# Optimization experiments

Measured on AMD Instinct MI355X. Metric: run time of the kernel, lower is better.

The kernel has to match this reference:

```python
import jax, jax.numpy as jnp
import numpy as np

B_SZ, SEQ, D_MODEL, D_STATE, KSIZE = 8, 4096, 1024, 64, 64
DT_MIN, DT_MAX = 0.001, 0.1


def setup_inputs() -> dict:
    key = jax.random.key(0)
    k1, k2, k3, k4 = jax.random.split(key, 4)
    u = jax.random.normal(k1, (B_SZ, SEQ, D_MODEL), dtype=jnp.float32)
    # HiPPO-like init: A = -(n+1)
    A = -(jnp.arange(D_STATE, dtype=jnp.float32) + 1.0)
    Bp = 0.01 * jax.random.normal(k2, (D_STATE, D_MODEL), dtype=jnp.float32)
    Cp = 0.01 * jax.random.normal(k3, (D_MODEL, D_STATE), dtype=jnp.float32)
    Dp = jnp.ones((D_MODEL,), dtype=jnp.float32)
    log_dt = jnp.log(jax.random.uniform(k4, (D_MODEL,), dtype=jnp.float32,
                                        minval=DT_MIN, maxval=DT_MAX))
    return {"u": u, "A": A, "B": Bp, "C": Cp, "D": Dp, "log_dt": log_dt}


def reference(u, A, B, C, D, log_dt):
    # u: (batch, seq_len, d_model)
    batch, seq_len, d_model = u.shape
    L = min(seq_len, KSIZE)  # truncated SSM kernel length

    # --- SSM kernel (same math as ssm_kernel) ---
    dt = jnp.exp(log_dt)                         # (d_model,)
    A_bar = jnp.exp(A[:, None] * dt[None, :])    # (d_state, d_model)
    powers = jnp.arange(L)[:, None, None]        # (L,1,1)
    A_powers = A_bar[None, :, :] ** powers       # (L, d_state, d_model)
    # K[l,k] = sum_{m,d} C[m,d] * A_bar[d,k]^l * B[d,k]  (faithful to original einsum)
    K = jnp.einsum('md,ldk,dk->lk', C, A_powers, B)  # (L, d_model)

    # --- Batched per-channel 'same' convolution via FFT ---
    # Equivalent to jnp.convolve(u[b,:,i], K[:,i], mode='same') for every b, i,
    # with L <= seq_len so the 'same' slice starts at (L-1)//2.
    n = seq_len + L - 1
    Uf = jnp.fft.rfft(u, n=n, axis=1)            # (batch, nf, d_model)
    Kf = jnp.fft.rfft(K, n=n, axis=0)            # (nf, d_model)
    conv_full = jnp.fft.irfft(Uf * Kf[None], n=n, axis=1)  # (batch, n, d_model)
    start = (L - 1) // 2
    y = conv_full[:, start:start + seq_len, :]

    # skip connection
    y = y + D[None, None, :] * u
    return y
```

## Files before the change

### kernel.cpp

```cpp
#include <hip/hip_runtime.h>

#define SEQ 4096
#define DM 1024
#define DS 64
#define KS 64

#define TCH 64
#define TT  64
#define R   8
#define NROW (TT + 64)

typedef const __attribute__((address_space(1))) void* gas_ptr;
typedef __attribute__((address_space(3))) void* las_ptr;
__device__ __forceinline__ void async_cp16(const void* g, void* s) {
    __builtin_amdgcn_global_load_lds((gas_ptr)g, (las_ptr)s, 16, 0, 0);
}

__global__ void csum_kernel(const float* __restrict__ C, float* __restrict__ csum) {
    int d    = threadIdx.x & 63;
    int mloc = threadIdx.x >> 6;
    int m0   = blockIdx.x * 64;
    float s = 0.f;
#pragma unroll
    for (int j = 0; j < 16; ++j)
        s += C[(m0 + j * 4 + mloc) * DS + d];
    __shared__ float red[4][64];
    red[mloc][d] = s;
    __syncthreads();
    if (threadIdx.x < 64) {
        float t = red[0][d] + red[1][d] + red[2][d] + red[3][d];
        atomicAdd(&csum[d], t);
    }
}

__global__ void taps_kernel(const float* __restrict__ A, const float* __restrict__ B,
                            const float* __restrict__ log_dt,
                            const float* __restrict__ csum, float* __restrict__ Ktl) {
    int g = blockIdx.x * blockDim.x + threadIdx.x;
    int k = g & (DM - 1);
    int l = g >> 10;
    float dt = __expf(log_dt[k]);
    float fl = (float)l;
    float acc = 0.f;
#pragma unroll 8
    for (int d = 0; d < DS; ++d)
        acc += csum[d] * __expf(A[d] * dt * fl) * B[d * DM + k];
    Ktl[g] = acc;
}

__global__ __launch_bounds__(256, 3)
void conv_kernel(const float* __restrict__ u, const float* __restrict__ Ktl,
                 const float* __restrict__ D, float* __restrict__ y) {
    __shared__ __align__(16) float smem_u[NROW * TCH];
    __shared__ __align__(16) float smem_t[KS * TCH];

    int k0 = blockIdx.x * TCH;
    int t0 = blockIdx.y * TT;
    int b  = blockIdx.z;

    int lane = threadIdx.x & 63;
    int wv   = threadIdx.x >> 6;

    const float* gt = u + (size_t)b * SEQ * DM + (size_t)(t0 - 32) * DM + k0;

    bool interior = (blockIdx.y > 0) && (blockIdx.y + 1 < SEQ / TT);

#pragma unroll
    for (int j = 0; j < 4; ++j) {
        int fb = j * 4096 + wv * 1024;
        int f  = fb + lane * 16;
        int l  = f >> 8;
        int c  = (f & 255) >> 2;
        async_cp16(Ktl + l * DM + k0 + c, (char*)smem_t + fb);
    }

    if (interior) {
#pragma unroll
        for (int j = 0; j < 8; ++j) {
            int fb = j * 4096 + wv * 1024;
            int f  = fb + lane * 16;
            int r  = f >> 8;
            int c  = (f & 255) >> 2;
            async_cp16(gt + (size_t)r * DM + c, (char*)smem_u + fb);
        }
    } else {
#pragma unroll
        for (int j = 0; j < 8; ++j) {
            int f = j * 4096 + threadIdx.x * 16;
            int r = f >> 8;
            int c = (f & 255) >> 2;
            int t = t0 - 32 + r;
            float4 v = make_float4(0.f, 0.f, 0.f, 0.f);
            if (t >= 0 && t < SEQ)
                v = *(const float4*)(gt + (size_t)r * DM + c);
            *(float4*)((char*)smem_u + f) = v;
        }
    }
    __syncthreads();

    int c2 = threadIdx.x & 31;
    int tg = threadIdx.x >> 5;
    int ts = t0 + tg * R;
    int rb = tg * R;

    const float2* us = (const float2*)smem_u;
    const float2* tp = (const float2*)smem_t;

    float2 acc[R];
#pragma unroll
    for (int r = 0; r < R; ++r) acc[r] = make_float2(0.f, 0.f);

    float2 D2 = *(const float2*)(D + k0 + 2 * c2);

    float2 w[16];
#pragma unroll
    for (int m = 55; m <= 70; ++m)
        w[m & 15] = us[(rb + m) * 32 + c2];

#pragma unroll
    for (int l = 0; l < 64; ++l) {
        float2 t2 = tp[l * 32 + c2];
#pragma unroll
        for (int r = 0; r < R; ++r) {
            float2 uv = w[(r + 63 - l) & 15];
            acc[r].x = fmaf(t2.x, uv.x, acc[r].x);
            acc[r].y = fmaf(t2.y, uv.y, acc[r].y);
        }
        if (l == 31) {
#pragma unroll
            for (int r = 0; r < R; ++r) {
                float2 uv = w[(r + 32) & 15];
                acc[r].x = fmaf(D2.x, uv.x, acc[r].x);
                acc[r].y = fmaf(D2.y, uv.y, acc[r].y);
            }
        }
        if (l <= 54) {
            int m = 54 - l;
            w[m & 15] = us[(rb + m) * 32 + c2];
        }
    }

    float2* yp2 = (float2*)y + (size_t)b * SEQ * (DM / 2) + (size_t)ts * (DM / 2) + (k0 >> 1) + c2;
#pragma unroll
    for (int r = 0; r < R; ++r)
        yp2[(size_t)r * (DM / 2)] = acc[r];
}

extern "C" void kernel_launch(void* const* d_in, const int* in_sizes, int n_in,
                              void* d_out, int out_size, void* d_ws, size_t ws_size,
                              hipStream_t stream) {
    const float* u      = (const float*)d_in[0];
    const float* A      = (const float*)d_in[1];
    const float* Bp     = (const float*)d_in[2];
    const float* Cp     = (const float*)d_in[3];
    const float* Dp     = (const float*)d_in[4];
    const float* log_dt = (const float*)d_in[5];
    float* y = (float*)d_out;

    float* csum = (float*)d_ws;
    float* Ktl  = csum + 64;

    hipMemsetAsync(csum, 0, DS * sizeof(float), stream);
    csum_kernel<<<16, 256, 0, stream>>>(Cp, csum);
    taps_kernel<<<(DM * KS) / 256, 256, 0, stream>>>(A, Bp, log_dt, csum, Ktl);

    dim3 grid(DM / TCH, SEQ / TT, 8);
    conv_kernel<<<grid, 256, 0, stream>>>(u, Ktl, Dp, y);
}
```

Baseline: 256.1 us.

## Process multiple time steps per block with a ring buffer and prefetch

```diff
diff --git a/kernel.cpp b/kernel.cpp
--- a/kernel.cpp
+++ b/kernel.cpp
@@ -6,9 +6,11 @@
 #define KS 64
 
 #define TCH 64
-#define TT  64
-#define R   8
-#define NROW (TT + 64)
+#define STEP 64
+#define NSTEP 8
+#define OUTB (STEP*NSTEP)
+#define R 8
+#define CAP 192
 
 typedef const __attribute__((address_space(1))) void* gas_ptr;
 typedef __attribute__((address_space(3))) void* las_ptr;
@@ -48,22 +50,20 @@
     Ktl[g] = acc;
 }
 
-__global__ __launch_bounds__(256, 3)
+__global__ __launch_bounds__(256, 2)
 void conv_kernel(const float* __restrict__ u, const float* __restrict__ Ktl,
                  const float* __restrict__ D, float* __restrict__ y) {
-    __shared__ __align__(16) float smem_u[NROW * TCH];
+    __shared__ __align__(16) float smem_u[CAP * TCH];
     __shared__ __align__(16) float smem_t[KS * TCH];
 
     int k0 = blockIdx.x * TCH;
-    int t0 = blockIdx.y * TT;
+    int ts = blockIdx.y * OUTB;
     int b  = blockIdx.z;
 
     int lane = threadIdx.x & 63;
     int wv   = threadIdx.x >> 6;
 
-    const float* gt = u + (size_t)b * SEQ * DM + (size_t)(t0 - 32) * DM + k0;
-
-    bool interior = (blockIdx.y > 0) && (blockIdx.y + 1 < SEQ / TT);
+    const float* ub = u + (size_t)b * SEQ * DM + k0;
 
 #pragma unroll
     for (int j = 0; j < 4; ++j) {
@@ -74,76 +74,132 @@
         async_cp16(Ktl + l * DM + k0 + c, (char*)smem_t + fb);
     }
 
-    if (interior) {
-#pragma unroll
-        for (int j = 0; j < 8; ++j) {
+    {
+        int A0 = ts - 32;
+        int sb0 = (A0 + 32) % CAP;
+        if (A0 >= 0) {
+#pragma unroll
+            for (int j = 0; j < 4; ++j) {
+                int fb = j * 4096 + wv * 1024;
+                int f  = fb + lane * 16;
+                int r  = f >> 8;
+                int c  = (f & 255) >> 2;
+                async_cp16(ub + (size_t)(A0 + r) * DM + c,
+                           (char*)smem_u + sb0 * 256 + fb);
+            }
+        } else {
+#pragma unroll
+            for (int j = 0; j < 4; ++j) {
+                int f = j * 4096 + threadIdx.x * 16;
+                int r = f >> 8;
+                int c = (f & 255) >> 2;
+                int t = A0 + r;
+                float4 v = make_float4(0.f, 0.f, 0.f, 0.f);
+                if (t >= 0)
+                    v = *(const float4*)(ub + (size_t)t * DM + c);
+                *(float4*)((char*)smem_u + sb0 * 256 + f) = v;
+            }
+        }
+        int A1 = ts + 32;
+        int sb1 = (A1 + 32) % CAP;
+#pragma unroll
+        for (int j = 0; j < 4; ++j) {
             int fb = j * 4096 + wv * 1024;
             int f  = fb + lane * 16;
             int r  = f >> 8;
             int c  = (f & 255) >> 2;
-            async_cp16(gt + (size_t)r * DM + c, (char*)smem_u + fb);
-        }
-    } else {
-#pragma unroll
-        for (int j = 0; j < 8; ++j) {
-            int f = j * 4096 + threadIdx.x * 16;
-            int r = f >> 8;
-            int c = (f & 255) >> 2;
-            int t = t0 - 32 + r;
-            float4 v = make_float4(0.f, 0.f, 0.f, 0.f);
-            if (t >= 0 && t < SEQ)
-                v = *(const float4*)(gt + (size_t)r * DM + c);
-            *(float4*)((char*)smem_u + f) = v;
+            async_cp16(ub + (size_t)(A1 + r) * DM + c,
+                       (char*)smem_u + sb1 * 256 + fb);
         }
     }
     __syncthreads();
 
     int c2 = threadIdx.x & 31;
     int tg = threadIdx.x >> 5;
-    int ts = t0 + tg * R;
-    int rb = tg * R;
 
     const float2* us = (const float2*)smem_u;
     const float2* tp = (const float2*)smem_t;
-
-    float2 acc[R];
-#pragma unroll
-    for (int r = 0; r < R; ++r) acc[r] = make_float2(0.f, 0.f);
-
     float2 D2 = *(const float2*)(D + k0 + 2 * c2);
 
-    float2 w[16];
-#pragma unroll
-    for (int m = 55; m <= 70; ++m)
-        w[m & 15] = us[(rb + m) * 32 + c2];
-
-#pragma unroll
-    for (int l = 0; l < 64; ++l) {
-        float2 t2 = tp[l * 32 + c2];
-#pragma unroll
-        for (int r = 0; r < R; ++r) {
-            float2 uv = w[(r + 63 - l) & 15];
-            acc[r].x = fmaf(t2.x, uv.x, acc[r].x);
-            acc[r].y = fmaf(t2.y, uv.y, acc[r].y);
-        }
-        if (l == 31) {
+    float2* yb = (float2*)y + (size_t)b * SEQ * (DM / 2) + (k0 >> 1) + c2;
+
+#pragma unroll 1
+    for (int s = 0; s < NSTEP; ++s) {
+        int t = ts + s * STEP;
+
+        if (s < NSTEP - 1) {
+            int A  = t + 96;
+            int sb = (A + 32) % CAP;
+            if (A + 63 < SEQ) {
+#pragma unroll
+                for (int j = 0; j < 4; ++j) {
+                    int fb = j * 4096 + wv * 1024;
+                    int f  = fb + lane * 16;
+                    int r  = f >> 8;
+                    int c  = (f & 255) >> 2;
+                    async_cp16(ub + (size_t)(A + r) * DM + c,
+                               (char*)smem_u + sb * 256 + fb);
+                }
+            } else {
+#pragma unroll
+                for (int j = 0; j < 4; ++j) {
+                    int f = j * 4096 + threadIdx.x * 16;
+                    int r = f >> 8;
+                    int c = (f & 255) >> 2;
+                    int tt = A + r;
+                    float4 v = make_float4(0.f, 0.f, 0.f, 0.f);
+                    if (tt < SEQ)
+                        v = *(const float4*)(ub + (size_t)tt * DM + c);
+                    *(float4*)((char*)smem_u + sb * 256 + f) = v;
+                }
+            }
+        }
+
+        int o0 = t + tg * R;
+
+        float2 acc[R];
+#pragma unroll
+        for (int r = 0; r < R; ++r) acc[r] = make_float2(0.f, 0.f);
+
+        float2 w[16];
+        int sl = (o0 + 55) % CAP;
+#pragma unroll
+        for (int m = 55; m <= 70; ++m) {
+            w[m & 15] = us[sl * 32 + c2];
+            sl = (sl == CAP - 1) ? 0 : sl + 1;
+        }
+        int sp = (o0 + 54) % CAP;
+
+#pragma unroll
+        for (int l = 0; l < 64; ++l) {
+            float2 t2 = tp[l * 32 + c2];
 #pragma unroll
             for (int r = 0; r < R; ++r) {
-                float2 uv = w[(r + 32) & 15];
-                acc[r].x = fmaf(D2.x, uv.x, acc[r].x);
-                acc[r].y = fmaf(D2.y, uv.y, acc[r].y);
-            }
-        }
-        if (l <= 54) {
-            int m = 54 - l;
-            w[m & 15] = us[(rb + m) * 32 + c2];
-        }
-    }
-
-    float2* yp2 = (float2*)y + (size_t)b * SEQ * (DM / 2) + (size_t)ts * (DM / 2) + (k0 >> 1) + c2;
-#pragma unroll
-    for (int r = 0; r < R; ++r)
-        yp2[(size_t)r * (DM / 2)] = acc[r];
+                float2 uv = w[(r + 63 - l) & 15];
+                acc[r].x = fmaf(t2.x, uv.x, acc[r].x);
+                acc[r].y = fmaf(t2.y, uv.y, acc[r].y);
+            }
+            if (l == 31) {
+#pragma unroll
+                for (int r = 0; r < R; ++r) {
+                    float2 uv = w[(r + 32) & 15];
+                    acc[r].x = fmaf(D2.x, uv.x, acc[r].x);
+                    acc[r].y = fmaf(D2.y, uv.y, acc[r].y);
+                }
+            }
+            if (l <= 54) {
+                w[(54 - l) & 15] = us[sp * 32 + c2];
+                sp = (sp == 0) ? CAP - 1 : sp - 1;
+            }
+        }
+
+        float2* yp = yb + (size_t)o0 * (DM / 2);
+#pragma unroll
+        for (int r = 0; r < R; ++r)
+            yp[(size_t)r * (DM / 2)] = acc[r];
+
+        __syncthreads();
+    }
 }
 
 extern "C" void kernel_launch(void* const* d_in, const int* in_sizes, int n_in,
@@ -164,6 +220,6 @@
     csum_kernel<<<16, 256, 0, stream>>>(Cp, csum);
     taps_kernel<<<(DM * KS) / 256, 256, 0, stream>>>(A, Bp, log_dt, csum, Ktl);
 
-    dim3 grid(DM / TCH, SEQ / TT, 8);
+    dim3 grid(DM / TCH, SEQ / OUTB, 8);
     conv_kernel<<<grid, 256, 0, stream>>>(u, Ktl, Dp, y);
 }
```

Result: slower. 272.0 us (+6.2%).

## Stream u directly from global memory instead of staging a halo tile in LDS

Applied to the files above, without the earlier changes.

```diff
diff --git a/kernel.cpp b/kernel.cpp
--- a/kernel.cpp
+++ b/kernel.cpp
@@ -8,7 +8,6 @@
 #define TCH 64
 #define TT  64
 #define R   8
-#define NROW (TT + 64)
 
 typedef const __attribute__((address_space(1))) void* gas_ptr;
 typedef __attribute__((address_space(3))) void* las_ptr;
@@ -48,74 +47,23 @@
     Ktl[g] = acc;
 }
 
-__global__ __launch_bounds__(256, 3)
-void conv_kernel(const float* __restrict__ u, const float* __restrict__ Ktl,
-                 const float* __restrict__ D, float* __restrict__ y) {
-    __shared__ __align__(16) float smem_u[NROW * TCH];
-    __shared__ __align__(16) float smem_t[KS * TCH];
-
-    int k0 = blockIdx.x * TCH;
-    int t0 = blockIdx.y * TT;
-    int b  = blockIdx.z;
-
-    int lane = threadIdx.x & 63;
-    int wv   = threadIdx.x >> 6;
-
-    const float* gt = u + (size_t)b * SEQ * DM + (size_t)(t0 - 32) * DM + k0;
-
-    bool interior = (blockIdx.y > 0) && (blockIdx.y + 1 < SEQ / TT);
-
-#pragma unroll
-    for (int j = 0; j < 4; ++j) {
-        int fb = j * 4096 + wv * 1024;
-        int f  = fb + lane * 16;
-        int l  = f >> 8;
-        int c  = (f & 255) >> 2;
-        async_cp16(Ktl + l * DM + k0 + c, (char*)smem_t + fb);
-    }
-
-    if (interior) {
-#pragma unroll
-        for (int j = 0; j < 8; ++j) {
-            int fb = j * 4096 + wv * 1024;
-            int f  = fb + lane * 16;
-            int r  = f >> 8;
-            int c  = (f & 255) >> 2;
-            async_cp16(gt + (size_t)r * DM + c, (char*)smem_u + fb);
-        }
-    } else {
-#pragma unroll
-        for (int j = 0; j < 8; ++j) {
-            int f = j * 4096 + threadIdx.x * 16;
-            int r = f >> 8;
-            int c = (f & 255) >> 2;
-            int t = t0 - 32 + r;
-            float4 v = make_float4(0.f, 0.f, 0.f, 0.f);
-            if (t >= 0 && t < SEQ)
-                v = *(const float4*)(gt + (size_t)r * DM + c);
-            *(float4*)((char*)smem_u + f) = v;
-        }
-    }
-    __syncthreads();
-
-    int c2 = threadIdx.x & 31;
-    int tg = threadIdx.x >> 5;
-    int ts = t0 + tg * R;
-    int rb = tg * R;
-
-    const float2* us = (const float2*)smem_u;
+template<bool GUARD>
+__device__ __forceinline__ void conv_compute(
+    const float* __restrict__ up,
+    const float* __restrict__ smem_t,
+    int c2, int o0, float2 D2, float2* acc)
+{
     const float2* tp = (const float2*)smem_t;
-
-    float2 acc[R];
-#pragma unroll
-    for (int r = 0; r < R; ++r) acc[r] = make_float2(0.f, 0.f);
-
-    float2 D2 = *(const float2*)(D + k0 + 2 * c2);
 
     float2 w[16];
 #pragma unroll
-    for (int m = 55; m <= 70; ++m)
-        w[m & 15] = us[(rb + m) * 32 + c2];
+    for (int m = 55; m <= 70; ++m) {
+        int a = m - 32;
+        float2 v = make_float2(0.f, 0.f);
+        if (!GUARD || ((unsigned)(o0 + a) < SEQ))
+            v = *(const float2*)(up + (ptrdiff_t)a * DM);
+        w[m & 15] = v;
+    }
 
 #pragma unroll
     for (int l = 0; l < 64; ++l) {
@@ -135,15 +83,58 @@
             }
         }
         if (l <= 54) {
-            int m = 54 - l;
-            w[m & 15] = us[(rb + m) * 32 + c2];
+            int a = 22 - l;
+            float2 v = make_float2(0.f, 0.f);
+            if (!GUARD || ((unsigned)(o0 + a) < SEQ))
+                v = *(const float2*)(up + (ptrdiff_t)a * DM);
+            w[(54 - l) & 15] = v;
         }
     }
+}
 
-    float2* yp2 = (float2*)y + (size_t)b * SEQ * (DM / 2) + (size_t)ts * (DM / 2) + (k0 >> 1) + c2;
+__global__ __launch_bounds__(256, 4)
+void conv_kernel(const float* __restrict__ u, const float* __restrict__ Ktl,
+                 const float* __restrict__ D, float* __restrict__ y) {
+    __shared__ __align__(16) float smem_t[KS * TCH];
+
+    int k0 = blockIdx.x * TCH;
+    int t0 = blockIdx.y * TT;
+    int b  = blockIdx.z;
+
+    int lane = threadIdx.x & 63;
+    int wv   = threadIdx.x >> 6;
+
+#pragma unroll
+    for (int j = 0; j < 4; ++j) {
+        int fb = j * 4096 + wv * 1024;
+        int f  = fb + lane * 16;
+        int l  = f >> 8;
+        int c  = (f & 255) >> 2;
+        async_cp16(Ktl + l * DM + k0 + c, (char*)smem_t + fb);
+    }
+    __syncthreads();
+
+    int c2 = threadIdx.x & 31;
+    int tg = threadIdx.x >> 5;
+    int o0 = t0 + tg * R;
+
+    const float* up = u + ((size_t)b * SEQ + o0) * DM + k0 + 2 * c2;
+    float2 D2 = *(const float2*)(D + k0 + 2 * c2);
+
+    float2 acc[R];
+#pragma unroll
+    for (int r = 0; r < R; ++r) acc[r] = make_float2(0.f, 0.f);
+
+    bool interior = (blockIdx.y > 0) && (blockIdx.y + 1 < SEQ / TT);
+    if (interior)
+        conv_compute<false>(up, smem_t, c2, o0, D2, acc);
+    else
+        conv_compute<true>(up, smem_t, c2, o0, D2, acc);
+
+    float2* yp = (float2*)y + ((size_t)b * SEQ + o0) * (DM / 2) + (k0 >> 1) + c2;
 #pragma unroll
     for (int r = 0; r < R; ++r)
-        yp2[(size_t)r * (DM / 2)] = acc[r];
+        yp[(size_t)r * (DM / 2)] = acc[r];
 }
 
 extern "C" void kernel_launch(void* const* d_in, const int* in_sizes, int n_in,
```

New measurement: 361.9 us. +41.3%, slower.

## Make conv blocks persistent over sequence steps with double-buffered LDS prefetch

Applied to the files above, without the earlier changes.

```diff
diff --git a/kernel.cpp b/kernel.cpp
--- a/kernel.cpp
+++ b/kernel.cpp
@@ -6,9 +6,11 @@
 #define KS 64
 
 #define TCH 64
-#define TT  64
-#define R   8
-#define NROW (TT + 64)
+#define STEP 64
+#define NSTEP 8
+#define OUTB (STEP*NSTEP)
+#define R 8
+#define NROW 128
 
 typedef const __attribute__((address_space(1))) void* gas_ptr;
 typedef __attribute__((address_space(3))) void* las_ptr;
@@ -48,22 +50,48 @@
     Ktl[g] = acc;
 }
 
-__global__ __launch_bounds__(256, 3)
+__device__ __forceinline__ void stage_tile(const float* __restrict__ ub, int a0,
+                                           char* dst, int lane, int wv, int tix,
+                                           bool guard) {
+    if (!guard) {
+#pragma unroll
+        for (int j = 0; j < 8; ++j) {
+            int fb = j * 4096 + wv * 1024;
+            int f  = fb + lane * 16;
+            int r  = f >> 8;
+            int c  = (f & 255) >> 2;
+            async_cp16(ub + (size_t)(a0 + r) * DM + c, dst + fb);
+        }
+    } else {
+#pragma unroll
+        for (int j = 0; j < 8; ++j) {
+            int f = j * 4096 + tix * 16;
+            int r = f >> 8;
+            int c = (f & 255) >> 2;
+            int a = a0 + r;
+            float4 v = make_float4(0.f, 0.f, 0.f, 0.f);
+            if ((unsigned)a < SEQ)
+                v = *(const float4*)(ub + (size_t)a * DM + c);
+            *(float4*)(dst + f) = v;
+        }
+    }
+}
+
+__global__ __launch_bounds__(256, 2)
 void conv_kernel(const float* __restrict__ u, const float* __restrict__ Ktl,
                  const float* __restrict__ D, float* __restrict__ y) {
-    __shared__ __align__(16) float smem_u[NROW * TCH];
+    __shared__ __align__(16) float smem_u[2 * NROW * TCH];
     __shared__ __align__(16) float smem_t[KS * TCH];
 
     int k0 = blockIdx.x * TCH;
-    int t0 = blockIdx.y * TT;
+    int ts = blockIdx.y * OUTB;
     int b  = blockIdx.z;
 
-    int lane = threadIdx.x & 63;
-    int wv   = threadIdx.x >> 6;
+    int tix  = threadIdx.x;
+    int lane = tix & 63;
+    int wv   = tix >> 6;
 
-    const float* gt = u + (size_t)b * SEQ * DM + (size_t)(t0 - 32) * DM + k0;
-
-    bool interior = (blockIdx.y > 0) && (blockIdx.y + 1 < SEQ / TT);
+    const float* ub = u + (size_t)b * SEQ * DM + k0;
 
 #pragma unroll
     for (int j = 0; j < 4; ++j) {
@@ -74,76 +102,70 @@
         async_cp16(Ktl + l * DM + k0 + c, (char*)smem_t + fb);
     }
 
-    if (interior) {
-#pragma unroll
-        for (int j = 0; j < 8; ++j) {
-            int fb = j * 4096 + wv * 1024;
-            int f  = fb + lane * 16;
-            int r  = f >> 8;
-            int c  = (f & 255) >> 2;
-            async_cp16(gt + (size_t)r * DM + c, (char*)smem_u + fb);
-        }
-    } else {
-#pragma unroll
-        for (int j = 0; j < 8; ++j) {
-            int f = j * 4096 + threadIdx.x * 16;
-            int r = f >> 8;
-            int c = (f & 255) >> 2;
-            int t = t0 - 32 + r;
-            float4 v = make_float4(0.f, 0.f, 0.f, 0.f);
-            if (t >= 0 && t < SEQ)
-                v = *(const float4*)(gt + (size_t)r * DM + c);
-            *(float4*)((char*)smem_u + f) = v;
-        }
-    }
+    stage_tile(ub, ts - 32, (char*)smem_u, lane, wv, tix, blockIdx.y == 0);
     __syncthreads();
 
-    int c2 = threadIdx.x & 31;
-    int tg = threadIdx.x >> 5;
-    int ts = t0 + tg * R;
+    int c2 = tix & 31;
+    int tg = tix >> 5;
     int rb = tg * R;
 
-    const float2* us = (const float2*)smem_u;
     const float2* tp = (const float2*)smem_t;
+    float2 D2 = *(const float2*)(D + k0 + 2 * c2);
+    float2* yb = (float2*)y + (size_t)b * SEQ * (DM / 2) + (k0 >> 1) + c2;
 
-    float2 acc[R];
+    int cur = 0;
+#pragma unroll 1
+    for (int s = 0; s < NSTEP; ++s) {
+        int t = ts + s * STEP;
+
+        if (s < NSTEP - 1) {
+            int a0n = t + 32;
+            stage_tile(ub, a0n, (char*)(smem_u + (cur ^ 1) * (NROW * TCH)),
+                       lane, wv, tix, a0n + NROW > SEQ);
+        }
+
+        const float2* usb = (const float2*)(smem_u + cur * (NROW * TCH));
+        int o0 = t + tg * R;
+
+        float2 acc[R];
 #pragma unroll
-    for (int r = 0; r < R; ++r) acc[r] = make_float2(0.f, 0.f);
+        for (int r = 0; r < R; ++r) acc[r] = make_float2(0.f, 0.f);
 
-    float2 D2 = *(const float2*)(D + k0 + 2 * c2);
-
-    float2 w[16];
+        float2 w[16];
 #pragma unroll
-    for (int m = 55; m <= 70; ++m)
-        w[m & 15] = us[(rb + m) * 32 + c2];
+        for (int m = 55; m <= 70; ++m)
+            w[m & 15] = usb[(rb + m) * 32 + c2];
 
 #pragma unroll
-    for (int l = 0; l < 64; ++l) {
-        float2 t2 = tp[l * 32 + c2];
-#pragma unroll
-        for (int r = 0; r < R; ++r) {
-            float2 uv = w[(r + 63 - l) & 15];
-            acc[r].x = fmaf(t2.x, uv.x, acc[r].x);
-            acc[r].y = fmaf(t2.y, uv.y, acc[r].y);
-        }
-        if (l == 31) {
+        for (int l = 0; l < 64; ++l) {
+            float2 t2 = tp[l * 32 + c2];
 #pragma unroll
             for (int r = 0; r < R; ++r) {
-                float2 uv = w[(r + 32) & 15];
-                acc[r].x = fmaf(D2.x, uv.x, acc[r].x);
-                acc[r].y = fmaf(D2.y, uv.y, acc[r].y);
+                float2 uv = w[(r + 63 - l) & 15];
+                acc[r].x = fmaf(t2.x, uv.x, acc[r].x);
+                acc[r].y = fmaf(t2.y, uv.y, acc[r].y);
+            }
+            if (l == 31) {
+#pragma unroll
+                for (int r = 0; r < R; ++r) {
+                    float2 uv = w[(r + 32) & 15];
+                    acc[r].x = fmaf(D2.x, uv.x, acc[r].x);
+                    acc[r].y = fmaf(D2.y, uv.y, acc[r].y);
+                }
+            }
+            if (l <= 54) {
+                w[(54 - l) & 15] = usb[(rb + 54 - l) * 32 + c2];
             }
         }
-        if (l <= 54) {
-            int m = 54 - l;
-            w[m & 15] = us[(rb + m) * 32 + c2];
-        }
+
+        float2* yp = yb + (size_t)o0 * (DM / 2);
+#pragma unroll
+        for (int r = 0; r < R; ++r)
+            yp[(size_t)r * (DM / 2)] = acc[r];
+
+        __syncthreads();
+        cur ^= 1;
     }
-
-    float2* yp2 = (float2*)y + (size_t)b * SEQ * (DM / 2) + (size_t)ts * (DM / 2) + (k0 >> 1) + c2;
-#pragma unroll
-    for (int r = 0; r < R; ++r)
-        yp2[(size_t)r * (DM / 2)] = acc[r];
 }
 
 extern "C" void kernel_launch(void* const* d_in, const int* in_sizes, int n_in,
@@ -164,6 +186,6 @@
     csum_kernel<<<16, 256, 0, stream>>>(Cp, csum);
     taps_kernel<<<(DM * KS) / 256, 256, 0, stream>>>(A, Bp, log_dt, csum, Ktl);
 
-    dim3 grid(DM / TCH, SEQ / TT, 8);
+    dim3 grid(DM / TCH, SEQ / OUTB, 8);
     conv_kernel<<<grid, 256, 0, stream>>>(u, Ktl, Dp, y);
 }
```

New measurement: 308.0 us. 1.2x slower.
